# Optimization experiments

Hardware: AMD Instinct MI355X
Metric: run time of the kernel (lower is better)

Reference implementation:

```python
import jax, jax.numpy as jnp
import numpy as np

SIZE_DICT = 512
DIM_DICT = 256
TEMPERATURE = 0.5
EPS = 1e-10


def setup_inputs() -> dict:
    key = jax.random.key(0)
    k1, k2, k3 = jax.random.split(key, 3)
    bs, dim_z, W, H = 32, DIM_DICT, 32, 32
    z_from_encoder = jax.random.normal(k1, (bs, dim_z, W, H), dtype=jnp.float32)
    kappa_q = jnp.ones((1,), dtype=jnp.float32)
    codebook = jax.random.normal(k2, (SIZE_DICT, DIM_DICT), dtype=jnp.float32)
    gumbel_u = jax.random.uniform(k3, (bs * W * H, SIZE_DICT), dtype=jnp.float32)
    return {"z_from_encoder": z_from_encoder, "kappa_q": kappa_q,
            "codebook": codebook, "gumbel_u": gumbel_u, "flg_train": 1}


def reference(z_from_encoder, kappa_q, codebook, gumbel_u, flg_train):
    bs, dim_z, W, H = z_from_encoder.shape
    # [bs, dim_z, W, H] -> [bs*W*H, dim_z]
    z_flat = jnp.transpose(z_from_encoder, (0, 2, 3, 1)).reshape(-1, dim_z)
    kq = jnp.clip(kappa_q, 1e-5, 1e5)  # scalar-ish [1]
    # L2-normalize codebook rows
    cb = codebook / jnp.linalg.norm(codebook, axis=1, keepdims=True)
    # logit = -distance = kappa * <z, c>   [N, K]
    logit = kq * (z_flat @ cb.T)
    logit = logit - jnp.max(logit, axis=-1, keepdims=True)
    logit = jnp.clip(logit, -50.0, 50.0)
    probabilities = jax.nn.softmax(logit, axis=-1)
    log_probabilities = jax.nn.log_softmax(logit, axis=-1)
    # training path: gumbel-softmax relaxation
    g = -jnp.log(-jnp.log(gumbel_u + EPS) + EPS)
    encodings = jax.nn.softmax((logit + g) / TEMPERATURE, axis=-1)
    z_quantized = (encodings @ cb).reshape(bs, W, H, dim_z)
    avg_probs = jnp.mean(jax.lax.stop_gradient(probabilities), axis=0)
    z_to_decoder = jnp.transpose(z_quantized, (0, 3, 1, 2))
    kld_discrete = jnp.sum(probabilities * log_probabilities) / bs
    kld_continuous = jnp.mean(
        jnp.sum(z_from_encoder * (z_from_encoder - z_to_decoder) * kq[0],
                axis=(1, 2, 3)))
    loss = kld_discrete + kld_continuous
    avg_probs = jnp.clip(avg_probs, 1e-10, None)
    perplexity = jnp.exp(-jnp.sum(avg_probs * jnp.log(avg_probs + 1e-10)))
    return z_to_decoder, loss, perplexity
```

## Files before the change

### kernel.cpp

```cpp
#include <hip/hip_runtime.h>
#include <stdint.h>


typedef float v4f __attribute__((ext_vector_type(4)));
typedef short v8s __attribute__((ext_vector_type(8)));
typedef short v4s __attribute__((ext_vector_type(4)));

#define ZA_STR 264
#define L2_STR 520

__device__ __forceinline__ uint16_t f2bf(float x) {
  uint32_t u = __float_as_uint(x);
  u = u + 0x7fffu + ((u >> 16) & 1u);
  return (uint16_t)(u >> 16);
}
__device__ __forceinline__ float bf2f(uint16_t h) {
  return __uint_as_float(((uint32_t)h) << 16);
}


__global__ __launch_bounds__(64) void vq_prep0(const float* __restrict__ cb,
                                               char* __restrict__ ws) {
  const int blk = blockIdx.x, t = threadIdx.x;
  float* shadow = (float*)(ws + 524288);
  float* scal   = (float*)(ws + 557056);
  float* rnorm  = (float*)(ws + 557072);
  if (blk < 512) {
    float s = 0.f;
#pragma unroll
    for (int i = 0; i < 4; i++) { const float v = cb[blk * 256 + t + 64 * i]; s += v * v; }
#pragma unroll
    for (int mm = 1; mm < 64; mm <<= 1) s += __shfl_xor(s, mm, 64);
    if (t == 0) rnorm[blk] = 1.0f / sqrtf(s);
  } else if (blk < 528) {
    const int j = blk - 512;
#pragma unroll
    for (int i = 0; i < 8; i++) shadow[j * 512 + t + 64 * i] = 0.f;
  } else {
    if (t < 3) scal[t] = 0.f;
  }
}

__global__ __launch_bounds__(256) void vq_prep1(const float* __restrict__ cb,
                                                char* __restrict__ ws) {
  const int b = blockIdx.x, t = threadIdx.x;
  uint16_t* cbn2 = (uint16_t*)ws;
  uint16_t* cbt2 = (uint16_t*)(ws + 262144);
  const float* rnorm = (const float*)(ws + 557072);
  union { v8s v; uint16_t u[8]; } pk;
  if (b < 64) {
    const int g = b * 256 + t;
    const int code = g >> 5, dch = g & 31;
    const float rn = rnorm[code];
    const float4 f0 = *(const float4*)(cb + code * 256 + dch * 8);
    const float4 f1 = *(const float4*)(cb + code * 256 + dch * 8 + 4);
    pk.u[0] = f2bf(f0.x * rn); pk.u[1] = f2bf(f0.y * rn);
    pk.u[2] = f2bf(f0.z * rn); pk.u[3] = f2bf(f0.w * rn);
    pk.u[4] = f2bf(f1.x * rn); pk.u[5] = f2bf(f1.y * rn);
    pk.u[6] = f2bf(f1.z * rn); pk.u[7] = f2bf(f1.w * rn);
    const int w = code >> 7, ct = (code >> 4) & 7, mcol = code & 15;
    const int ks = dch >> 2, q3 = dch & 3;
    *(v8s*)(cbn2 + ((ks * 8 + ct) * 4 + w) * 512 + (q3 * 16 + mcol) * 8) = pk.v;
  } else {
    const int g = (b - 64) * 256 + t;
    const int cgroup = g >> 8, d = g & 255;
#pragma unroll
    for (int j = 0; j < 8; j++) {
      const int c = cgroup * 8 + j;
      pk.u[j] = f2bf(cb[c * 256 + d] * rnorm[c]);
    }
    const int cc = cgroup >> 2, qq = cgroup & 3;
    const int wd = d >> 6, nt = (d >> 4) & 3, md = d & 15;
    *(v8s*)(cbt2 + ((cc * 4 + nt) * 4 + wd) * 512 + (qq * 16 + md) * 8) = pk.v;
  }
}

__global__ __launch_bounds__(256, 4) void vq_main(const float* __restrict__ z,
                                                  const float* __restrict__ kappa,
                                                  const float* __restrict__ gum,
                                                  char* __restrict__ ws,
                                                  float* __restrict__ out) {
  __shared__ char s_A[33280];
  __shared__ float s_pm[128], s_pS[128], s_pT[128];
  __shared__ float s_M[32], s_rS[32], s_kd[32], s_rSe[32], s_red[8];

  const int t = threadIdx.x;
  const int w = t >> 6, lane = t & 63, q = lane >> 4, m = lane & 15;
  const int bi = blockIdx.x, b = bi >> 5, wh0 = (bi & 31) << 5;
  const int R0 = bi << 5;

  const uint16_t* cbn2 = (const uint16_t*)ws;
  const uint16_t* cbt2 = (const uint16_t*)(ws + 262144);
  float* shadow = (float*)(ws + 524288);
  float* scal   = (float*)(ws + 557056);

  uint16_t* za  = (uint16_t*)s_A;
  uint16_t* l2s = (uint16_t*)s_A;

  const float kq = fminf(fmaxf(kappa[0], 1e-5f), 1e5f);

  const int row = t >> 3, c4 = (t & 7) << 2;
  const float* gbase = gum + (size_t)(R0 + row) * 512 + c4;

  {
    float zs = 0.f;
    const int whb = (t & 7) << 2, dT = t >> 3;
    const float* zb = z + ((size_t)b << 18) + wh0 + whb;
#pragma unroll
    for (int s = 0; s < 8; s++) {
      const int d = dT + (s << 5);
      const float4 v = *(const float4*)(zb + (d << 10));
      zs += v.x * v.x + v.y * v.y + v.z * v.z + v.w * v.w;
      za[(whb + 0) * ZA_STR + d] = f2bf(v.x);
      za[(whb + 1) * ZA_STR + d] = f2bf(v.y);
      za[(whb + 2) * ZA_STR + d] = f2bf(v.z);
      za[(whb + 3) * ZA_STR + d] = f2bf(v.w);
    }
#pragma unroll
    for (int mm = 1; mm < 64; mm <<= 1) zs += __shfl_xor(zs, mm, 64);
    if (lane == 0) s_red[w] = zs;
  }

  float4 gq[4];
#pragma unroll
  for (int i = 0; i < 4; i++) gq[i] = *(const float4*)(gbase + (i << 5));

  __syncthreads();
  if (t == 0) atomicAdd(&scal[1], s_red[0] + s_red[1] + s_red[2] + s_red[3]);

  v4f acc0[8], acc1[8];
#pragma unroll
  for (int i = 0; i < 8; i++) { acc0[i] = (v4f)0.f; acc1[i] = (v4f)0.f; }
  {
    const uint16_t* bp  = cbn2 + (w << 9) + (lane << 3);
    const uint16_t* a0p = za + m * ZA_STR;
    const uint16_t* a1p = za + (m + 16) * ZA_STR;
#pragma unroll
    for (int ks = 0; ks < 8; ks++) {
      const v8s a0 = *(const v8s*)(a0p + (ks << 5) + (q << 3));
      const v8s a1 = *(const v8s*)(a1p + (ks << 5) + (q << 3));
#pragma unroll
      for (int ct = 0; ct < 8; ct++) {
        const v8s bf = *(const v8s*)(bp + (((ks << 3) + ct) << 11));
        acc0[ct] = __builtin_amdgcn_mfma_f32_16x16x32_bf16(a0, bf, acc0[ct], 0, 0, 0);
        acc1[ct] = __builtin_amdgcn_mfma_f32_16x16x32_bf16(a1, bf, acc1[ct], 0, 0, 0);
      }
    }
  }
#pragma unroll
  for (int i = 0; i < 8; i++) { acc0[i] *= kq; acc1[i] *= kq; }

  {
    auto stats_half = [&](v4f (&acc)[8], int half) {
#pragma unroll
      for (int reg = 0; reg < 4; reg++) {
        float mx = -1e30f;
#pragma unroll
        for (int ct = 0; ct < 8; ct++) mx = fmaxf(mx, acc[ct][reg]);
#pragma unroll
        for (int mm = 1; mm < 16; mm <<= 1) mx = fmaxf(mx, __shfl_xor(mx, mm, 64));
        float S = 0.f, T = 0.f;
#pragma unroll
        for (int ct = 0; ct < 8; ct++) {
          const float d = acc[ct][reg] - mx;
          const float e = __expf(d);
          S += e; T += d * e;
        }
#pragma unroll
        for (int mm = 1; mm < 16; mm <<= 1) { S += __shfl_xor(S, mm, 64); T += __shfl_xor(T, mm, 64); }
        if (m == 0) {
          const int r = half * 16 + q * 4 + reg;
          s_pm[(w << 5) + r] = mx; s_pS[(w << 5) + r] = S; s_pT[(w << 5) + r] = T;
        }
      }
    };
    stats_half(acc0, 0);
    stats_half(acc1, 1);
  }
  __syncthreads();
  if (t < 32) {
    float M = s_pm[t];
    M = fmaxf(M, s_pm[32 + t]); M = fmaxf(M, s_pm[64 + t]); M = fmaxf(M, s_pm[96 + t]);
    float S = 0.f, T = 0.f;
#pragma unroll
    for (int ww = 0; ww < 4; ww++) {
      const float dm = s_pm[ww * 32 + t] - M;
      const float al = __expf(dm);
      S += s_pS[ww * 32 + t] * al;
      T += (s_pT[ww * 32 + t] + dm * s_pS[ww * 32 + t]) * al;
    }
    const float rS = 1.0f / S;
    s_M[t] = M; s_rS[t] = rS; s_kd[t] = T * rS - __logf(S);
  }
  __syncthreads();

  {
    const int c0 = w << 7;
    float colacc[8];
#pragma unroll
    for (int i = 0; i < 8; i++) colacc[i] = 0.f;
    auto pass2_half = [&](v4f (&acc)[8], int half) {
#pragma unroll
      for (int reg = 0; reg < 4; reg++) {
        const int r = half * 16 + q * 4 + reg;
        const float Mr = s_M[r], rSr = s_rS[r];
        uint16_t* lrow = l2s + r * L2_STR + c0 + m;
#pragma unroll
        for (int ct = 0; ct < 8; ct++) {
          const float d = fmaxf(acc[ct][reg] - Mr, -50.0f);
          const float e = __expf(d);
          colacc[ct] += e * rSr;
          lrow[ct << 4] = f2bf(e);
        }
      }
    };
    pass2_half(acc0, 0);
    pass2_half(acc1, 1);
#pragma unroll
    for (int i = 0; i < 8; i++) {
      colacc[i] += __shfl_xor(colacc[i], 16, 64);
      colacc[i] += __shfl_xor(colacc[i], 32, 64);
    }
    if (q == 0) {
      float* sh = shadow + ((bi & 15) << 9) + c0 + m;
#pragma unroll
      for (int i = 0; i < 8; i++) atomicAdd(&sh[i << 4], colacc[i]);
    }
    if (w == 0) {
      float kd = s_kd[lane & 31];
#pragma unroll
      for (int mm = 1; mm < 64; mm <<= 1) kd += __shfl_xor(kd, mm, 64);
      if (lane == 0) atomicAdd(&scal[0], 0.5f * kd);
    }
  }
  __syncthreads();

  {
    const float mxr = s_M[row];
    float se = 0.f, ce = 0.f;
    union { v4s v; uint16_t h[4]; } ev, rv;
#pragma unroll
    for (int i = 0; i < 16; i++) {
      const float4 u = gq[i & 3];
      const float uu[4] = {u.x, u.y, u.z, u.w};
      ev.v = *(const v4s*)(l2s + row * L2_STR + (i << 5) + c4);
      if (i < 12) gq[i & 3] = *(const float4*)(gbase + ((i + 4) << 5));
#pragma unroll
      for (int j = 0; j < 4; j++) {
        const float e = bf2f(ev.h[j]);
        const float L = -__logf(uu[j] + 1e-10f) + 1e-10f;
        const float f = __fdividef(e, L);
        const float er = f * f;
        se += er;
        ce += er * (__logf(e) + mxr);
        rv.h[j] = f2bf(er);
      }
      *(v4s*)(l2s + row * L2_STR + (i << 5) + c4) = rv.v;
    }
#pragma unroll
    for (int mm = 1; mm < 8; mm <<= 1) { se += __shfl_xor(se, mm, 64); ce += __shfl_xor(ce, mm, 64); }
    float cr = ((t & 7) == 0) ? (ce / se) : 0.f;
#pragma unroll
    for (int mm = 8; mm < 64; mm <<= 1) cr += __shfl_xor(cr, mm, 64);
    if (lane == 0) s_red[w] = cr;
    if ((t & 7) == 0) s_rSe[row] = 1.0f / se;
  }
  __syncthreads();
  if (t == 0) atomicAdd(&scal[2], s_red[0] + s_red[1] + s_red[2] + s_red[3]);

  v4f acc2a[4], acc2b[4];
#pragma unroll
  for (int i = 0; i < 4; i++) { acc2a[i] = (v4f)0.f; acc2b[i] = (v4f)0.f; }
  {
    const uint16_t* a0p = l2s + m * L2_STR;
    const uint16_t* a1p = l2s + (m + 16) * L2_STR;
#pragma unroll
    for (int cc = 0; cc < 16; cc++) {
      const v8s a0 = *(const v8s*)(a0p + (cc << 5) + (q << 3));
      const v8s a1 = *(const v8s*)(a1p + (cc << 5) + (q << 3));
      const uint16_t* bp2 = cbt2 + (cc << 13) + (w << 9) + (lane << 3);
#pragma unroll
      for (int nt = 0; nt < 4; nt++) {
        const v8s bf = *(const v8s*)(bp2 + (nt << 11));
        acc2a[nt] = __builtin_amdgcn_mfma_f32_16x16x32_bf16(a0, bf, acc2a[nt], 0, 0, 0);
        acc2b[nt] = __builtin_amdgcn_mfma_f32_16x16x32_bf16(a1, bf, acc2b[nt], 0, 0, 0);
      }
    }
  }

  {
    float* ob = out + ((size_t)b << 18) + wh0;
    const int d0 = w << 6;
    float rsA[4], rsB[4];
#pragma unroll
    for (int reg = 0; reg < 4; reg++) {
      rsA[reg] = s_rSe[q * 4 + reg];
      rsB[reg] = s_rSe[16 + q * 4 + reg];
    }
#pragma unroll
    for (int nt = 0; nt < 4; nt++) {
      const int d = d0 + (nt << 4) + m;
#pragma unroll
      for (int reg = 0; reg < 4; reg++) {
        ob[(d << 10) + q * 4 + reg]      = acc2a[nt][reg] * rsA[reg];
        ob[(d << 10) + 16 + q * 4 + reg] = acc2b[nt][reg] * rsB[reg];
      }
    }
  }
}

__global__ __launch_bounds__(512) void vq_final(const float* __restrict__ kappa,
                                                char* __restrict__ ws,
                                                float* __restrict__ out) {
  __shared__ float red[8];
  const int t = threadIdx.x;
  const float* shadow = (const float*)(ws + 524288);
  const float* scal   = (const float*)(ws + 557056);
  float s = 0.f;
#pragma unroll
  for (int j = 0; j < 16; j++) s += shadow[(j << 9) + t];
  float avg = fmaxf(s * (1.0f / 32768.0f), 1e-10f);
  float term = avg * __logf(avg + 1e-10f);
#pragma unroll
  for (int mm = 1; mm < 64; mm <<= 1) term += __shfl_xor(term, mm, 64);
  if ((t & 63) == 0) red[t >> 6] = term;
  __syncthreads();
  if (t == 0) {
    float H = 0.f;
#pragma unroll
    for (int i = 0; i < 8; i++) H += red[i];
    const float perpl = __expf(-H);
    const float kq = fminf(fmaxf(kappa[0], 1e-5f), 1e5f);
    const float loss = (scal[0] + kq * scal[1] - scal[2]) * (1.0f / 32.0f);
    out[8388608] = loss;
    out[8388609] = perpl;
  }
}

extern "C" void kernel_launch(void* const* d_in, const int* in_sizes, int n_in,
                              void* d_out, int out_size, void* d_ws, size_t ws_size,
                              hipStream_t stream) {
  const float* z     = (const float*)d_in[0];
  const float* kappa = (const float*)d_in[1];
  const float* cb    = (const float*)d_in[2];
  const float* gum   = (const float*)d_in[3];
  char* ws = (char*)d_ws;
  float* out = (float*)d_out;
  hipLaunchKernelGGL(vq_prep0, dim3(529),  dim3(64),  0, stream, cb, ws);
  hipLaunchKernelGGL(vq_prep1, dim3(128),  dim3(256), 0, stream, cb, ws);
  hipLaunchKernelGGL(vq_main,  dim3(1024), dim3(256), 0, stream, z, kappa, gum, ws, out);
  hipLaunchKernelGGL(vq_final, dim3(1),    dim3(512), 0, stream, kappa, ws, out);
}
```

Measured before the change: 200.6 us.

## Merge prep kernels, fold kappa into codebook, fuse Gumbel pass into softmax pass

The two codebook prep kernels become one, which computes row norms in shared memory, zeroes the accumulators, and multiplies kappa into the normalized codebook so the main kernel no longer scales its logits. In the main kernel the Gumbel-softmax weights are now computed directly from the MFMA accumulators in the same loop as the softmax. This removes a separate pass that re-read bf16 probabilities from LDS and recomputed a log. Gumbel noise is loaded in a transposed pattern with a double buffer, and the column and KL atomics are moved after the output stores. In exchange, the Gumbel loads become scalar rather than float4, and the kernel needs more shared memory.

```diff
diff --git a/kernel.cpp b/kernel.cpp
--- a/kernel.cpp
+++ b/kernel.cpp
@@ -14,46 +14,34 @@
   u = u + 0x7fffu + ((u >> 16) & 1u);
   return (uint16_t)(u >> 16);
 }
-__device__ __forceinline__ float bf2f(uint16_t h) {
-  return __uint_as_float(((uint32_t)h) << 16);
-}
-
-
-__global__ __launch_bounds__(64) void vq_prep0(const float* __restrict__ cb,
+
+
+__global__ __launch_bounds__(256) void vq_prep(const float* __restrict__ cb,
+                                               const float* __restrict__ kappa,
                                                char* __restrict__ ws) {
-  const int blk = blockIdx.x, t = threadIdx.x;
-  float* shadow = (float*)(ws + 524288);
-  float* scal   = (float*)(ws + 557056);
-  float* rnorm  = (float*)(ws + 557072);
-  if (blk < 512) {
-    float s = 0.f;
-#pragma unroll
-    for (int i = 0; i < 4; i++) { const float v = cb[blk * 256 + t + 64 * i]; s += v * v; }
-#pragma unroll
-    for (int mm = 1; mm < 64; mm <<= 1) s += __shfl_xor(s, mm, 64);
-    if (t == 0) rnorm[blk] = 1.0f / sqrtf(s);
-  } else if (blk < 528) {
-    const int j = blk - 512;
-#pragma unroll
-    for (int i = 0; i < 8; i++) shadow[j * 512 + t + 64 * i] = 0.f;
-  } else {
-    if (t < 3) scal[t] = 0.f;
-  }
-}
-
-__global__ __launch_bounds__(256) void vq_prep1(const float* __restrict__ cb,
-                                                char* __restrict__ ws) {
   const int b = blockIdx.x, t = threadIdx.x;
   uint16_t* cbn2 = (uint16_t*)ws;
   uint16_t* cbt2 = (uint16_t*)(ws + 262144);
-  const float* rnorm = (const float*)(ws + 557072);
+  float* shadow  = (float*)(ws + 524288);
+  float* scal    = (float*)(ws + 557056);
+  __shared__ float s_rn[8];
+
+  const int cbase = (b & 63) << 3;
+  const int cl = t >> 5, lt = t & 31;
+  const float4 f0 = *(const float4*)(cb + (cbase + cl) * 256 + lt * 8);
+  const float4 f1 = *(const float4*)(cb + (cbase + cl) * 256 + lt * 8 + 4);
+  float s = f0.x*f0.x + f0.y*f0.y + f0.z*f0.z + f0.w*f0.w
+          + f1.x*f1.x + f1.y*f1.y + f1.z*f1.z + f1.w*f1.w;
+#pragma unroll
+  for (int mm = 1; mm < 32; mm <<= 1) s += __shfl_xor(s, mm, 64);
+  if (lt == 0) s_rn[cl] = 1.0f / sqrtf(s);
+  __syncthreads();
+
   union { v8s v; uint16_t u[8]; } pk;
   if (b < 64) {
-    const int g = b * 256 + t;
-    const int code = g >> 5, dch = g & 31;
-    const float rn = rnorm[code];
-    const float4 f0 = *(const float4*)(cb + code * 256 + dch * 8);
-    const float4 f1 = *(const float4*)(cb + code * 256 + dch * 8 + 4);
+    const float kq = fminf(fmaxf(kappa[0], 1e-5f), 1e5f);
+    const int code = cbase + cl, dch = lt;
+    const float rn = s_rn[cl] * kq;
     pk.u[0] = f2bf(f0.x * rn); pk.u[1] = f2bf(f0.y * rn);
     pk.u[2] = f2bf(f0.z * rn); pk.u[3] = f2bf(f0.w * rn);
     pk.u[4] = f2bf(f1.x * rn); pk.u[5] = f2bf(f1.y * rn);
@@ -62,27 +50,29 @@
     const int ks = dch >> 2, q3 = dch & 3;
     *(v8s*)(cbn2 + ((ks * 8 + ct) * 4 + w) * 512 + (q3 * 16 + mcol) * 8) = pk.v;
   } else {
-    const int g = (b - 64) * 256 + t;
-    const int cgroup = g >> 8, d = g & 255;
+    const int cgroup = b - 64, d = t;
 #pragma unroll
     for (int j = 0; j < 8; j++) {
-      const int c = cgroup * 8 + j;
-      pk.u[j] = f2bf(cb[c * 256 + d] * rnorm[c]);
+      const int c = cbase + j;
+      pk.u[j] = f2bf(cb[c * 256 + d] * s_rn[j]);
     }
     const int cc = cgroup >> 2, qq = cgroup & 3;
     const int wd = d >> 6, nt = (d >> 4) & 3, md = d & 15;
     *(v8s*)(cbt2 + ((cc * 4 + nt) * 4 + wd) * 512 + (qq * 16 + md) * 8) = pk.v;
+    if (t < 128) shadow[(cgroup << 7) + t] = 0.f;
+    if (cgroup == 0 && t >= 128 && t < 131) scal[t - 128] = 0.f;
   }
 }
 
 __global__ __launch_bounds__(256, 4) void vq_main(const float* __restrict__ z,
-                                                  const float* __restrict__ kappa,
                                                   const float* __restrict__ gum,
                                                   char* __restrict__ ws,
                                                   float* __restrict__ out) {
   __shared__ char s_A[33280];
   __shared__ float s_pm[128], s_pS[128], s_pT[128];
   __shared__ float s_M[32], s_rS[32], s_kd[32], s_rSe[32], s_red[8];
+  __shared__ float s_se[128], s_ce[128];
+  __shared__ float s_col[512];
 
   const int t = threadIdx.x;
   const int w = t >> 6, lane = t & 63, q = lane >> 4, m = lane & 15;
@@ -96,11 +86,6 @@
 
   uint16_t* za  = (uint16_t*)s_A;
   uint16_t* l2s = (uint16_t*)s_A;
-
-  const float kq = fminf(fmaxf(kappa[0], 1e-5f), 1e5f);
-
-  const int row = t >> 3, c4 = (t & 7) << 2;
-  const float* gbase = gum + (size_t)(R0 + row) * 512 + c4;
 
   {
     float zs = 0.f;
@@ -120,11 +105,6 @@
     for (int mm = 1; mm < 64; mm <<= 1) zs += __shfl_xor(zs, mm, 64);
     if (lane == 0) s_red[w] = zs;
   }
-
-  float4 gq[4];
-#pragma unroll
-  for (int i = 0; i < 4; i++) gq[i] = *(const float4*)(gbase + (i << 5));
-
   __syncthreads();
   if (t == 0) atomicAdd(&scal[1], s_red[0] + s_red[1] + s_red[2] + s_red[3]);
 
@@ -147,8 +127,6 @@
       }
     }
   }
-#pragma unroll
-  for (int i = 0; i < 8; i++) { acc0[i] *= kq; acc1[i] *= kq; }
 
   {
     auto stats_half = [&](v4f (&acc)[8], int half) {
@@ -177,6 +155,14 @@
     stats_half(acc0, 0);
     stats_half(acc1, 1);
   }
+
+  const float* gT = gum + (((size_t)R0 + (q << 2)) << 9) + (w << 7) + m;
+  float gb[2][8];
+#pragma unroll
+  for (int ct = 0; ct < 8; ct++) gb[0][ct] = gT[ct << 4];
+#pragma unroll
+  for (int ct = 0; ct < 8; ct++) gb[1][ct] = gT[512 + (ct << 4)];
+
   __syncthreads();
   if (t < 32) {
     float M = s_pm[t];
@@ -199,74 +185,60 @@
     float colacc[8];
 #pragma unroll
     for (int i = 0; i < 8; i++) colacc[i] = 0.f;
-    auto pass2_half = [&](v4f (&acc)[8], int half) {
-#pragma unroll
-      for (int reg = 0; reg < 4; reg++) {
-        const int r = half * 16 + q * 4 + reg;
-        const float Mr = s_M[r], rSr = s_rS[r];
-        uint16_t* lrow = l2s + r * L2_STR + c0 + m;
-#pragma unroll
-        for (int ct = 0; ct < 8; ct++) {
-          const float d = fmaxf(acc[ct][reg] - Mr, -50.0f);
-          const float e = __expf(d);
-          colacc[ct] += e * rSr;
-          lrow[ct << 4] = f2bf(e);
-        }
-      }
-    };
-    pass2_half(acc0, 0);
-    pass2_half(acc1, 1);
+#pragma unroll
+    for (int g = 0; g < 8; g++) {
+      const int h = g >> 2, rg = g & 3;
+      const int r = (h << 4) + (q << 2) + rg;
+      const float Mr = s_M[r], rSr = s_rS[r];
+      uint16_t* lrow = l2s + r * L2_STR + c0 + m;
+      float se = 0.f, ce = 0.f;
+#pragma unroll
+      for (int ct = 0; ct < 8; ct++) {
+        const float a = h ? acc1[ct][rg] : acc0[ct][rg];
+        const float d = fmaxf(a - Mr, -50.0f);
+        const float e = __expf(d);
+        colacc[ct] += e * rSr;
+        const float L = 1e-10f - __logf(gb[g & 1][ct] + 1e-10f);
+        const float f = __fdividef(e, L);
+        const float er = f * f;
+        se += er;
+        ce += er * (d + Mr);
+        lrow[ct << 4] = f2bf(er);
+      }
+      if (g < 6) {
+        const int g2 = g + 2;
+        const int off = (((g2 >> 2) << 4) + (g2 & 3)) << 9;
+#pragma unroll
+        for (int ct = 0; ct < 8; ct++) gb[g & 1][ct] = gT[off + (ct << 4)];
+      }
+#pragma unroll
+      for (int mm = 1; mm < 16; mm <<= 1) {
+        se += __shfl_xor(se, mm, 64);
+        ce += __shfl_xor(ce, mm, 64);
+      }
+      if (m == 0) { s_se[(w << 5) + r] = se; s_ce[(w << 5) + r] = ce; }
+    }
 #pragma unroll
     for (int i = 0; i < 8; i++) {
       colacc[i] += __shfl_xor(colacc[i], 16, 64);
       colacc[i] += __shfl_xor(colacc[i], 32, 64);
     }
     if (q == 0) {
-      float* sh = shadow + ((bi & 15) << 9) + c0 + m;
-#pragma unroll
-      for (int i = 0; i < 8; i++) atomicAdd(&sh[i << 4], colacc[i]);
-    }
-    if (w == 0) {
-      float kd = s_kd[lane & 31];
-#pragma unroll
-      for (int mm = 1; mm < 64; mm <<= 1) kd += __shfl_xor(kd, mm, 64);
-      if (lane == 0) atomicAdd(&scal[0], 0.5f * kd);
-    }
-  }
-  __syncthreads();
-
-  {
-    const float mxr = s_M[row];
-    float se = 0.f, ce = 0.f;
-    union { v4s v; uint16_t h[4]; } ev, rv;
-#pragma unroll
-    for (int i = 0; i < 16; i++) {
-      const float4 u = gq[i & 3];
-      const float uu[4] = {u.x, u.y, u.z, u.w};
-      ev.v = *(const v4s*)(l2s + row * L2_STR + (i << 5) + c4);
-      if (i < 12) gq[i & 3] = *(const float4*)(gbase + ((i + 4) << 5));
-#pragma unroll
-      for (int j = 0; j < 4; j++) {
-        const float e = bf2f(ev.h[j]);
-        const float L = -__logf(uu[j] + 1e-10f) + 1e-10f;
-        const float f = __fdividef(e, L);
-        const float er = f * f;
-        se += er;
-        ce += er * (__logf(e) + mxr);
-        rv.h[j] = f2bf(er);
-      }
-      *(v4s*)(l2s + row * L2_STR + (i << 5) + c4) = rv.v;
-    }
-#pragma unroll
-    for (int mm = 1; mm < 8; mm <<= 1) { se += __shfl_xor(se, mm, 64); ce += __shfl_xor(ce, mm, 64); }
-    float cr = ((t & 7) == 0) ? (ce / se) : 0.f;
-#pragma unroll
-    for (int mm = 8; mm < 64; mm <<= 1) cr += __shfl_xor(cr, mm, 64);
-    if (lane == 0) s_red[w] = cr;
-    if ((t & 7) == 0) s_rSe[row] = 1.0f / se;
-  }
-  __syncthreads();
-  if (t == 0) atomicAdd(&scal[2], s_red[0] + s_red[1] + s_red[2] + s_red[3]);
+#pragma unroll
+      for (int i = 0; i < 8; i++) s_col[c0 + (i << 4) + m] = colacc[i];
+    }
+  }
+  __syncthreads();
+
+  if (t < 32) {
+    const float se = s_se[t] + s_se[32 + t] + s_se[64 + t] + s_se[96 + t];
+    const float ce = s_ce[t] + s_ce[32 + t] + s_ce[64 + t] + s_ce[96 + t];
+    s_rSe[t] = 1.0f / se;
+    float cr = ce / se;
+#pragma unroll
+    for (int mm = 1; mm < 32; mm <<= 1) cr += __shfl_xor(cr, mm, 64);
+    if (t == 0) atomicAdd(&scal[2], cr);
+  }
 
   v4f acc2a[4], acc2b[4];
 #pragma unroll
@@ -287,6 +259,7 @@
       }
     }
   }
+  __syncthreads();
 
   {
     float* ob = out + ((size_t)b << 18) + wh0;
@@ -305,6 +278,18 @@
         ob[(d << 10) + q * 4 + reg]      = acc2a[nt][reg] * rsA[reg];
         ob[(d << 10) + 16 + q * 4 + reg] = acc2b[nt][reg] * rsB[reg];
       }
+    }
+  }
+
+  {
+    float* sh = shadow + ((bi & 15) << 9);
+    atomicAdd(&sh[t], s_col[t]);
+    atomicAdd(&sh[256 + t], s_col[256 + t]);
+    if (w == 0) {
+      float kd = s_kd[lane & 31];
+#pragma unroll
+      for (int mm = 1; mm < 64; mm <<= 1) kd += __shfl_xor(kd, mm, 64);
+      if (lane == 0) atomicAdd(&scal[0], 0.5f * kd);
     }
   }
 }
@@ -346,8 +331,7 @@
   const float* gum   = (const float*)d_in[3];
   char* ws = (char*)d_ws;
   float* out = (float*)d_out;
-  hipLaunchKernelGGL(vq_prep0, dim3(529),  dim3(64),  0, stream, cb, ws);
-  hipLaunchKernelGGL(vq_prep1, dim3(128),  dim3(256), 0, stream, cb, ws);
-  hipLaunchKernelGGL(vq_main,  dim3(1024), dim3(256), 0, stream, z, kappa, gum, ws, out);
+  hipLaunchKernelGGL(vq_prep,  dim3(128),  dim3(256), 0, stream, cb, kappa, ws);
+  hipLaunchKernelGGL(vq_main,  dim3(1024), dim3(256), 0, stream, z, gum, ws, out);
   hipLaunchKernelGGL(vq_final, dim3(1),    dim3(512), 0, stream, kappa, ws, out);
 }
```

Result: faster. 186.3 us (-7.1%).
